# Performance work log

Measured on AMD Instinct MI355X. Metric: run time of the kernel, lower is better.

## Reference

```python
import jax, jax.numpy as jnp
import numpy as np

N_NODES = 100000
N_EDGES = 500000
D_IN = 128
D_HID = 128
D_OUT = 128


def _sage_conv(x, src, dst, W_l, b_l, W_r, n_nodes):
    # mean aggregation of source-node features at destination nodes
    msg = jax.ops.segment_sum(x[src], dst, num_segments=n_nodes)          # [N, d_in]
    cnt = jax.ops.segment_sum(jnp.ones((src.shape[0], 1), x.dtype), dst,
                              num_segments=n_nodes)                        # [N, 1]
    agg = msg / jnp.maximum(cnt, 1.0)
    # PyG SAGEConv: lin_l(aggregated) + lin_r(self), bias on lin_l only
    return agg @ W_l + b_l + x @ W_r


def setup_inputs() -> dict:
    key = jax.random.key(0)
    ks = jax.random.split(key, 8)
    x = jax.random.normal(ks[0], (N_NODES, D_IN), dtype=jnp.float32)
    edge_index = jax.random.randint(ks[1], (2, N_EDGES), 0, N_NODES, dtype=jnp.int32)
    s1 = 1.0 / np.sqrt(D_IN)
    s2 = 1.0 / np.sqrt(D_HID)
    W_l1 = jax.random.uniform(ks[2], (D_IN, D_HID), jnp.float32, -s1, s1)
    W_r1 = jax.random.uniform(ks[3], (D_IN, D_HID), jnp.float32, -s1, s1)
    b_l1 = jnp.zeros((D_HID,), jnp.float32)
    W_l2 = jax.random.uniform(ks[4], (D_HID, D_OUT), jnp.float32, -s2, s2)
    W_r2 = jax.random.uniform(ks[5], (D_HID, D_OUT), jnp.float32, -s2, s2)
    b_l2 = jnp.zeros((D_OUT,), jnp.float32)
    return {"x": x, "edge_index": edge_index,
            "W_l1": W_l1, "b_l1": b_l1, "W_r1": W_r1,
            "W_l2": W_l2, "b_l2": b_l2, "W_r2": W_r2}


def reference(x, edge_index, W_l1, b_l1, W_r1, W_l2, b_l2, W_r2):
    src, dst = edge_index[0], edge_index[1]
    h = _sage_conv(x, src, dst, W_l1, b_l1, W_r1, N_NODES)
    h = jax.nn.relu(h)
    out = _sage_conv(h, src, dst, W_l2, b_l2, W_r2, N_NODES)
    return out
```

## Files before the change

### kernel.cpp

```cpp
#include <hip/hip_runtime.h>
#include <cstddef>

#define N_NODES 100000
#define N_EDGES 500000
#define D 128

typedef __attribute__((ext_vector_type(8))) short bf16x8;
typedef __attribute__((ext_vector_type(4))) float f32x4;

static __device__ __forceinline__ short f2bf(float f)
{
    unsigned u = __builtin_bit_cast(unsigned, f);
    unsigned r = (u + 0x7fffu + ((u >> 16) & 1u)) >> 16;
    return (short)r;
}


__global__ __launch_bounds__(256)
void hist_kernel(const int* __restrict__ dst, int* __restrict__ deg)
{
    int e = blockIdx.x * 256 + threadIdx.x;
    if (e < N_EDGES) atomicAdd(&deg[dst[e]], 1);
}

__global__ __launch_bounds__(512)
void scanA_kernel(const int* __restrict__ deg, int* __restrict__ bsum)
{
    __shared__ int s[512];
    int t = threadIdx.x;
    int idx = blockIdx.x * 512 + t;
    s[t] = (idx < N_NODES) ? deg[idx] : 0;
    __syncthreads();
    for (int off = 256; off > 0; off >>= 1) {
        if (t < off) s[t] += s[t + off];
        __syncthreads();
    }
    if (t == 0) bsum[blockIdx.x] = s[0];
}

__global__ __launch_bounds__(256)
void scanB_kernel(const int* __restrict__ bsum, int* __restrict__ boff)
{
    __shared__ int s[256];
    int t = threadIdx.x;
    int v = (t < 196) ? bsum[t] : 0;
    s[t] = v;
    __syncthreads();
    for (int off = 1; off < 256; off <<= 1) {
        int a = s[t];
        if (t >= off) a += s[t - off];
        __syncthreads();
        s[t] = a;
        __syncthreads();
    }
    if (t < 196) boff[t] = s[t] - v;
}

__global__ __launch_bounds__(512)
void scanC_kernel(const int* __restrict__ deg, const int* __restrict__ boff,
                  int* __restrict__ row_ptr, int* __restrict__ cursor)
{
    __shared__ int s[512];
    int t = threadIdx.x;
    int idx = blockIdx.x * 512 + t;
    int v = (idx < N_NODES) ? deg[idx] : 0;
    s[t] = v;
    __syncthreads();
    for (int off = 1; off < 512; off <<= 1) {
        int a = s[t];
        if (t >= off) a += s[t - off];
        __syncthreads();
        s[t] = a;
        __syncthreads();
    }
    int excl = boff[blockIdx.x] + s[t] - v;
    if (idx < N_NODES) { row_ptr[idx] = excl; cursor[idx] = excl; }
    else if (idx == N_NODES) { row_ptr[idx] = excl; }
}

__global__ __launch_bounds__(256)
void permute_kernel(const int* __restrict__ src, const int* __restrict__ dst,
                    int* __restrict__ cursor, int* __restrict__ perm)
{
    int e = blockIdx.x * 256 + threadIdx.x;
    if (e < N_EDGES) {
        int pos = atomicAdd(&cursor[dst[e]], 1);
        perm[pos] = src[e];
    }
}

__global__ __launch_bounds__(256)
void gather_kernel(const float* __restrict__ x,
                   const int* __restrict__ row_ptr,
                   const int* __restrict__ perm,
                   float* __restrict__ agg)
{
    unsigned gid = blockIdx.x * 256 + threadIdx.x;
    unsigned node = gid >> 5;
    unsigned c4 = (gid & 31) << 2;
    if (node >= N_NODES) return;
    int beg = row_ptr[node];
    int end = row_ptr[node + 1];
    float4 acc = make_float4(0.f, 0.f, 0.f, 0.f);
    int e = beg;
    for (; e + 4 <= end; e += 4) {
        int s0 = perm[e + 0], s1 = perm[e + 1], s2 = perm[e + 2], s3 = perm[e + 3];
        float4 v0 = *reinterpret_cast<const float4*>(x + (size_t)s0 * D + c4);
        float4 v1 = *reinterpret_cast<const float4*>(x + (size_t)s1 * D + c4);
        float4 v2 = *reinterpret_cast<const float4*>(x + (size_t)s2 * D + c4);
        float4 v3 = *reinterpret_cast<const float4*>(x + (size_t)s3 * D + c4);
        acc.x += (v0.x + v1.x) + (v2.x + v3.x);
        acc.y += (v0.y + v1.y) + (v2.y + v3.y);
        acc.z += (v0.z + v1.z) + (v2.z + v3.z);
        acc.w += (v0.w + v1.w) + (v2.w + v3.w);
    }
    for (; e < end; ++e) {
        int s0 = perm[e];
        float4 v0 = *reinterpret_cast<const float4*>(x + (size_t)s0 * D + c4);
        acc.x += v0.x; acc.y += v0.y; acc.z += v0.z; acc.w += v0.w;
    }
    float inv = 1.0f / fmaxf((float)(end - beg), 1.0f);
    acc.x *= inv; acc.y *= inv; acc.z *= inv; acc.w *= inv;
    *reinterpret_cast<float4*>(agg + (size_t)node * D + c4) = acc;
}

__global__ __launch_bounds__(256)
void pack_w_kernel(const float* __restrict__ Wl, const float* __restrict__ Wr,
                   short* __restrict__ blob)
{
    int tid = blockIdx.x * 256 + threadIdx.x;
    if (tid >= 4096) return;
    int lane = tid & 63;
    int frag = tid >> 6;
    int cb = frag & 7;
    int ks = frag >> 3;
    int k0 = ks * 32 + (lane >> 4) * 8;
    int col = cb * 16 + (lane & 15);
    const float* W = (k0 < 128) ? (Wl + (size_t)k0 * D) : (Wr + (size_t)(k0 - 128) * D);
    bf16x8 v;
    #pragma unroll
    for (int j = 0; j < 8; ++j)
        v[j] = f2bf(W[(size_t)j * D + col]);
    *reinterpret_cast<bf16x8*>(blob + (size_t)tid * 8) = v;
}

__global__ __launch_bounds__(256)
void mfma_gemm_kernel(const float* __restrict__ aggf,
                      const float* __restrict__ selff,
                      const short* __restrict__ blob,
                      const float* __restrict__ bias,
                      float* __restrict__ out,
                      int relu)
{
    const int tid = threadIdx.x;
    const int w = tid >> 6;
    const int lane = tid & 63;
    const int kch = lane >> 4;
    int row = blockIdx.x * 64 + w * 16 + (lane & 15);
    int rowc = row < N_NODES ? row : N_NODES - 1;

    const float* aggp = aggf + (size_t)rowc * D + kch * 8;
    const float* selfp = selff + (size_t)rowc * D + kch * 8;

    f32x4 acc[8] = {};

    #pragma unroll
    for (int ks = 0; ks < 8; ++ks) {
        const float* src = (ks < 4) ? (aggp + ks * 32) : (selfp + (ks - 4) * 32);
        float4 lo = *reinterpret_cast<const float4*>(src);
        float4 hi = *reinterpret_cast<const float4*>(src + 4);
        bf16x8 a;
        a[0] = f2bf(lo.x); a[1] = f2bf(lo.y); a[2] = f2bf(lo.z); a[3] = f2bf(lo.w);
        a[4] = f2bf(hi.x); a[5] = f2bf(hi.y); a[6] = f2bf(hi.z); a[7] = f2bf(hi.w);
        const short* bptr = blob + ((size_t)(ks * 8) * 64 + lane) * 8;
        #pragma unroll
        for (int cb = 0; cb < 8; ++cb) {
            bf16x8 b = *reinterpret_cast<const bf16x8*>(bptr + (size_t)cb * 64 * 8);
            acc[cb] = __builtin_amdgcn_mfma_f32_16x16x32_bf16(a, b, acc[cb], 0, 0, 0);
        }
    }

    const int colg = lane & 15;
    const int rbase = blockIdx.x * 64 + w * 16 + (lane >> 4) * 4;
    #pragma unroll
    for (int cb = 0; cb < 8; ++cb) {
        int col = cb * 16 + colg;
        float bv = bias[col];
        #pragma unroll
        for (int r = 0; r < 4; ++r) {
            int rr = rbase + r;
            if (rr < N_NODES) {
                float v = acc[cb][r] + bv;
                if (relu) v = fmaxf(v, 0.0f);
                out[(size_t)rr * D + col] = v;
            }
        }
    }
}

extern "C" void kernel_launch(void* const* d_in, const int* in_sizes, int n_in,
                              void* d_out, int out_size, void* d_ws, size_t ws_size,
                              hipStream_t stream)
{
    const float* x   = (const float*)d_in[0];
    const int*   ei  = (const int*)d_in[1];
    const int*   src = ei;
    const int*   dst = ei + N_EDGES;
    const float* Wl1 = (const float*)d_in[2];
    const float* bl1 = (const float*)d_in[3];
    const float* Wr1 = (const float*)d_in[4];
    const float* Wl2 = (const float*)d_in[5];
    const float* bl2 = (const float*)d_in[6];
    const float* Wr2 = (const float*)d_in[7];
    float* out = (float*)d_out;

    int* deg     = (int*)d_ws;
    int* row_ptr = deg + N_NODES;
    int* cursor  = row_ptr + N_NODES + 1;
    int* bsum    = cursor + N_NODES;
    int* boff    = bsum + 256;
    int* perm    = boff + 256;
    size_t int_end = (size_t)(3 * N_NODES + 1 + 512) + N_EDGES;
    int_end = (int_end + 3) & ~(size_t)3;
    short* blob1 = (short*)((int*)d_ws + int_end);
    short* blob2 = blob1 + 32768;
    float* agg   = (float*)(blob2 + 32768);

    const int edge_blocks = (N_EDGES + 255) / 256;
    const int scan_blocks = (N_NODES + 512) / 512;
    const int gath_blocks = (N_NODES * 32) / 256;
    const int gemm_blocks = (N_NODES + 63) / 64;

    hipMemsetAsync(deg, 0, N_NODES * sizeof(int), stream);
    hist_kernel<<<edge_blocks, 256, 0, stream>>>(dst, deg);
    scanA_kernel<<<scan_blocks, 512, 0, stream>>>(deg, bsum);
    scanB_kernel<<<1, 256, 0, stream>>>(bsum, boff);
    scanC_kernel<<<scan_blocks, 512, 0, stream>>>(deg, boff, row_ptr, cursor);
    permute_kernel<<<edge_blocks, 256, 0, stream>>>(src, dst, cursor, perm);
    pack_w_kernel<<<16, 256, 0, stream>>>(Wl1, Wr1, blob1);
    pack_w_kernel<<<16, 256, 0, stream>>>(Wl2, Wr2, blob2);

    gather_kernel<<<gath_blocks, 256, 0, stream>>>(x, row_ptr, perm, agg);
    mfma_gemm_kernel<<<gemm_blocks, 256, 0, stream>>>(agg, x, blob1, bl1, out, 1);

    gather_kernel<<<gath_blocks, 256, 0, stream>>>(out, row_ptr, perm, agg);
    mfma_gemm_kernel<<<gemm_blocks, 256, 0, stream>>>(agg, out, blob2, bl2, out, 0);
}
```

Before: 321.7 us.

## Store node features and aggregates in bf16 to halve gather traffic

Adds a cast kernel that converts x to bf16 once. The gather kernel now reads bf16 rows with 16 threads per node and writes a bf16 aggregate. The first-layer GEMM writes its ReLU output as bf16 in place over the cast buffer, and both GEMMs load bf16 operands directly instead of converting fp32 on the fly. This halves the bytes moved by the random-access neighbour gathers and the GEMM input loads, at the cost of an extra cast pass and bf16 rounding before neighbour summation. The two weight-packing launches are also merged into one.

New measurement: 296.1 us. -8.0%, faster.

```diff
diff --git a/kernel.cpp b/kernel.cpp
--- a/kernel.cpp
+++ b/kernel.cpp
@@ -13,6 +13,10 @@
     unsigned u = __builtin_bit_cast(unsigned, f);
     unsigned r = (u + 0x7fffu + ((u >> 16) & 1u)) >> 16;
     return (short)r;
+}
+static __device__ __forceinline__ float b2f(short s)
+{
+    return __builtin_bit_cast(float, (unsigned)((unsigned short)s) << 16);
 }
 
 
@@ -90,52 +94,67 @@
 }
 
 __global__ __launch_bounds__(256)
-void gather_kernel(const float* __restrict__ x,
+void cast_kernel(const float* __restrict__ in, short* __restrict__ outb)
+{
+    int i = blockIdx.x * 256 + threadIdx.x;
+    const float4* p = reinterpret_cast<const float4*>(in) + (size_t)i * 2;
+    float4 lo = p[0], hi = p[1];
+    bf16x8 v;
+    v[0] = f2bf(lo.x); v[1] = f2bf(lo.y); v[2] = f2bf(lo.z); v[3] = f2bf(lo.w);
+    v[4] = f2bf(hi.x); v[5] = f2bf(hi.y); v[6] = f2bf(hi.z); v[7] = f2bf(hi.w);
+    *reinterpret_cast<bf16x8*>(outb + (size_t)i * 8) = v;
+}
+
+__global__ __launch_bounds__(256)
+void gather_kernel(const short* __restrict__ xb,
                    const int* __restrict__ row_ptr,
                    const int* __restrict__ perm,
-                   float* __restrict__ agg)
+                   short* __restrict__ aggb)
 {
     unsigned gid = blockIdx.x * 256 + threadIdx.x;
-    unsigned node = gid >> 5;
-    unsigned c4 = (gid & 31) << 2;
+    unsigned node = gid >> 4;
+    unsigned c8 = (gid & 15) << 3;
     if (node >= N_NODES) return;
     int beg = row_ptr[node];
     int end = row_ptr[node + 1];
-    float4 acc = make_float4(0.f, 0.f, 0.f, 0.f);
+    float acc[8] = {};
     int e = beg;
-    for (; e + 4 <= end; e += 4) {
-        int s0 = perm[e + 0], s1 = perm[e + 1], s2 = perm[e + 2], s3 = perm[e + 3];
-        float4 v0 = *reinterpret_cast<const float4*>(x + (size_t)s0 * D + c4);
-        float4 v1 = *reinterpret_cast<const float4*>(x + (size_t)s1 * D + c4);
-        float4 v2 = *reinterpret_cast<const float4*>(x + (size_t)s2 * D + c4);
-        float4 v3 = *reinterpret_cast<const float4*>(x + (size_t)s3 * D + c4);
-        acc.x += (v0.x + v1.x) + (v2.x + v3.x);
-        acc.y += (v0.y + v1.y) + (v2.y + v3.y);
-        acc.z += (v0.z + v1.z) + (v2.z + v3.z);
-        acc.w += (v0.w + v1.w) + (v2.w + v3.w);
-    }
-    for (; e < end; ++e) {
+    for (; e + 2 <= end; e += 2) {
+        int s0 = perm[e], s1 = perm[e + 1];
+        bf16x8 v0 = *reinterpret_cast<const bf16x8*>(xb + (size_t)s0 * D + c8);
+        bf16x8 v1 = *reinterpret_cast<const bf16x8*>(xb + (size_t)s1 * D + c8);
+        #pragma unroll
+        for (int j = 0; j < 8; ++j) acc[j] += b2f(v0[j]) + b2f(v1[j]);
+    }
+    if (e < end) {
         int s0 = perm[e];
-        float4 v0 = *reinterpret_cast<const float4*>(x + (size_t)s0 * D + c4);
-        acc.x += v0.x; acc.y += v0.y; acc.z += v0.z; acc.w += v0.w;
+        bf16x8 v0 = *reinterpret_cast<const bf16x8*>(xb + (size_t)s0 * D + c8);
+        #pragma unroll
+        for (int j = 0; j < 8; ++j) acc[j] += b2f(v0[j]);
     }
     float inv = 1.0f / fmaxf((float)(end - beg), 1.0f);
-    acc.x *= inv; acc.y *= inv; acc.z *= inv; acc.w *= inv;
-    *reinterpret_cast<float4*>(agg + (size_t)node * D + c4) = acc;
-}
-
-__global__ __launch_bounds__(256)
-void pack_w_kernel(const float* __restrict__ Wl, const float* __restrict__ Wr,
+    bf16x8 o;
+    #pragma unroll
+    for (int j = 0; j < 8; ++j) o[j] = f2bf(acc[j] * inv);
+    *reinterpret_cast<bf16x8*>(aggb + (size_t)node * D + c8) = o;
+}
+
+__global__ __launch_bounds__(256)
+void pack_w_kernel(const float* __restrict__ Wl1, const float* __restrict__ Wr1,
+                   const float* __restrict__ Wl2, const float* __restrict__ Wr2,
                    short* __restrict__ blob)
 {
     int tid = blockIdx.x * 256 + threadIdx.x;
-    if (tid >= 4096) return;
+    if (tid >= 8192) return;
     int lane = tid & 63;
-    int frag = tid >> 6;
+    int frag = (tid >> 6) & 63;
+    int layer = tid >> 12;
     int cb = frag & 7;
     int ks = frag >> 3;
     int k0 = ks * 32 + (lane >> 4) * 8;
     int col = cb * 16 + (lane & 15);
+    const float* Wl = layer ? Wl2 : Wl1;
+    const float* Wr = layer ? Wr2 : Wr1;
     const float* W = (k0 < 128) ? (Wl + (size_t)k0 * D) : (Wr + (size_t)(k0 - 128) * D);
     bf16x8 v;
     #pragma unroll
@@ -145,12 +164,13 @@
 }
 
 __global__ __launch_bounds__(256)
-void mfma_gemm_kernel(const float* __restrict__ aggf,
-                      const float* __restrict__ selff,
+void mfma_gemm_kernel(const short* __restrict__ aggb,
+                      const short* __restrict__ selfb,
                       const short* __restrict__ blob,
                       const float* __restrict__ bias,
-                      float* __restrict__ out,
-                      int relu)
+                      float* __restrict__ outf,
+                      short* __restrict__ outb,
+                      int mode)
 {
     const int tid = threadIdx.x;
     const int w = tid >> 6;
@@ -159,19 +179,15 @@
     int row = blockIdx.x * 64 + w * 16 + (lane & 15);
     int rowc = row < N_NODES ? row : N_NODES - 1;
 
-    const float* aggp = aggf + (size_t)rowc * D + kch * 8;
-    const float* selfp = selff + (size_t)rowc * D + kch * 8;
+    const short* aggp = aggb + (size_t)rowc * D + kch * 8;
+    const short* selfp = selfb + (size_t)rowc * D + kch * 8;
 
     f32x4 acc[8] = {};
 
     #pragma unroll
     for (int ks = 0; ks < 8; ++ks) {
-        const float* src = (ks < 4) ? (aggp + ks * 32) : (selfp + (ks - 4) * 32);
-        float4 lo = *reinterpret_cast<const float4*>(src);
-        float4 hi = *reinterpret_cast<const float4*>(src + 4);
-        bf16x8 a;
-        a[0] = f2bf(lo.x); a[1] = f2bf(lo.y); a[2] = f2bf(lo.z); a[3] = f2bf(lo.w);
-        a[4] = f2bf(hi.x); a[5] = f2bf(hi.y); a[6] = f2bf(hi.z); a[7] = f2bf(hi.w);
+        const short* src = (ks < 4) ? (aggp + ks * 32) : (selfp + (ks - 4) * 32);
+        bf16x8 a = *reinterpret_cast<const bf16x8*>(src);
         const short* bptr = blob + ((size_t)(ks * 8) * 64 + lane) * 8;
         #pragma unroll
         for (int cb = 0; cb < 8; ++cb) {
@@ -191,8 +207,12 @@
             int rr = rbase + r;
             if (rr < N_NODES) {
                 float v = acc[cb][r] + bv;
-                if (relu) v = fmaxf(v, 0.0f);
-                out[(size_t)rr * D + col] = v;
+                if (mode) {
+                    v = fmaxf(v, 0.0f);
+                    outb[(size_t)rr * D + col] = f2bf(v);
+                } else {
+                    outf[(size_t)rr * D + col] = v;
+                }
             }
         }
     }
@@ -224,11 +244,13 @@
     int_end = (int_end + 3) & ~(size_t)3;
     short* blob1 = (short*)((int*)d_ws + int_end);
     short* blob2 = blob1 + 32768;
-    float* agg   = (float*)(blob2 + 32768);
+    short* xb    = blob2 + 32768;
+    short* aggb  = xb + (size_t)N_NODES * D;
 
     const int edge_blocks = (N_EDGES + 255) / 256;
     const int scan_blocks = (N_NODES + 512) / 512;
-    const int gath_blocks = (N_NODES * 32) / 256;
+    const int cast_blocks = (N_NODES * D / 8) / 256;
+    const int gath_blocks = (N_NODES * 16) / 256;
     const int gemm_blocks = (N_NODES + 63) / 64;
 
     hipMemsetAsync(deg, 0, N_NODES * sizeof(int), stream);
@@ -237,12 +259,14 @@
     scanB_kernel<<<1, 256, 0, stream>>>(bsum, boff);
     scanC_kernel<<<scan_blocks, 512, 0, stream>>>(deg, boff, row_ptr, cursor);
     permute_kernel<<<edge_blocks, 256, 0, stream>>>(src, dst, cursor, perm);
-    pack_w_kernel<<<16, 256, 0, stream>>>(Wl1, Wr1, blob1);
-    pack_w_kernel<<<16, 256, 0, stream>>>(Wl2, Wr2, blob2);
-
-    gather_kernel<<<gath_blocks, 256, 0, stream>>>(x, row_ptr, perm, agg);
-    mfma_gemm_kernel<<<gemm_blocks, 256, 0, stream>>>(agg, x, blob1, bl1, out, 1);
-
-    gather_kernel<<<gath_blocks, 256, 0, stream>>>(out, row_ptr, perm, agg);
-    mfma_gemm_kernel<<<gemm_blocks, 256, 0, stream>>>(agg, out, blob2, bl2, out, 0);
-}
+    cast_kernel<<<cast_blocks, 256, 0, stream>>>(x, xb);
+    pack_w_kernel<<<32, 256, 0, stream>>>(Wl1, Wr1, Wl2, Wr2, blob1);
+
+    gather_kernel<<<gath_blocks, 256, 0, stream>>>(xb, row_ptr, perm, aggb);
+    mfma_gemm_kernel<<<gemm_blocks, 256, 0, stream>>>(aggb, xb, blob1, bl1,
+                                                      nullptr, xb, 1);
+
+    gather_kernel<<<gath_blocks, 256, 0, stream>>>(xb, row_ptr, perm, aggb);
+    mfma_gemm_kernel<<<gemm_blocks, 256, 0, stream>>>(aggb, xb, blob2, bl2,
+                                                      out, nullptr, 0);
+}
```
